# Optimization experiments

Hardware: AMD Instinct MI355X
Metric: run time of the kernel (lower is better)

Reference implementation:

```python
import jax, jax.numpy as jnp
import numpy as np

BATCH, SEQ, DMODEL, NSTATE = 4, 2048, 1024, 16


def setup_inputs() -> dict:
    key = jax.random.key(0)
    ks = jax.random.split(key, 6)
    def lin_w(k, out_d, in_d):
        # torch Linear default init scale ~ 1/sqrt(in_d)
        return jax.random.uniform(k, (out_d, in_d), jnp.float32, -1.0, 1.0) / np.sqrt(in_d).astype(np.float32)
    return {
        "x": jax.random.normal(ks[0], (BATCH, SEQ, DMODEL), jnp.float32),
        "W1": lin_w(ks[1], DMODEL, DMODEL), "b1": jnp.zeros((DMODEL,), jnp.float32),
        "W2": lin_w(ks[2], NSTATE, DMODEL), "b2": jnp.zeros((NSTATE,), jnp.float32),
        "W3": lin_w(ks[3], NSTATE, DMODEL), "b3": jnp.zeros((NSTATE,), jnp.float32),
        # A: xavier_uniform over (d_model, state_size)
        "A": jax.random.uniform(ks[4], (DMODEL, NSTATE), jnp.float32, -1.0, 1.0) * np.sqrt(6.0 / (DMODEL + NSTATE)).astype(np.float32),
    }


def reference(x, W1, b1, W2, b2, W3, b3, A):
    # Projections (bld -> bln / bld)
    Bmat = x @ W2.T + b2                      # (b, l, n)
    Cmat = x @ W3.T + b3                      # (b, l, n)
    delta = jax.nn.softplus(x @ W1.T + b1)    # (b, l, d)
    # Original math (flag=0 path):
    #   dB[b,l,d,n] = delta[b,l,d] * B[b,l,n]
    #   dA = exp(einsum('bld,dn->bldn', delta, A))  -- multiplied by a zeros h, so it
    #        contributes nothing to the output (dead math; A receives zero grad).
    #   h  = dA * 0 + x[...,None] * dB
    #   y  = einsum('bln,bldn->bld', C, h)
    # This reduces exactly to: y = x * delta * sum_n(B * C)
    bc = jnp.einsum('bln,bln->bl', Bmat, Cmat)  # (b, l)
    y = x * delta * bc[..., None]               # (b, l, d)
    return y
```

## Files before the change

kernel.cpp:

```cpp
#include <hip/hip_runtime.h>
#include <hip/hip_bf16.h>
#include <cmath>

#define BATCH 4
#define SEQ 2048
#define DM 1024
#define NS 16
#define M_ROWS (BATCH * SEQ)

typedef short bf16x8 __attribute__((ext_vector_type(8)));
typedef short bf16x4 __attribute__((ext_vector_type(4)));
typedef float f32x4 __attribute__((ext_vector_type(4)));

__device__ __forceinline__ short f2bf(float f) {
    union { float f; unsigned u; } a; a.f = f;
    unsigned u = a.u;
    return (short)((u + 0x7fffu + ((u >> 16) & 1u)) >> 16);
}
__device__ __forceinline__ float bf2f(unsigned short s) {
    union { unsigned u; float f; } a; a.u = ((unsigned)s) << 16;
    return a.f;
}

#define LDS_CAST(p) ((__attribute__((address_space(3))) unsigned*)(p))
#define GLB_CAST(p) ((const __attribute__((address_space(1))) unsigned*)(p))

__global__ void __launch_bounds__(256) convert_all(
    const float* __restrict__ x,  const float* __restrict__ W1,
    const float* __restrict__ W2, const float* __restrict__ W3,
    short* __restrict__ xb, short* __restrict__ W1b, short* __restrict__ Wcb)
{
    const int b = blockIdx.x;
    const int t = threadIdx.x;
    const float4* src; bf16x4* dst; int qbase;
    if (b < 2048)      { src = (const float4*)x;  dst = (bf16x4*)xb;  qbase = b * 1024; }
    else if (b < 2304) { src = (const float4*)W1; dst = (bf16x4*)W1b; qbase = (b - 2048) * 1024; }
    else if (b < 2308) { src = (const float4*)W2; dst = (bf16x4*)Wcb; qbase = (b - 2304) * 1024; }
    else               { src = (const float4*)W3; dst = (bf16x4*)(Wcb + NS * DM); qbase = (b - 2308) * 1024; }
    #pragma unroll
    for (int i = 0; i < 4; i++) {
        int q = qbase + i * 256 + t;
        float4 v = src[q];
        bf16x4 s;
        s.x = f2bf(v.x); s.y = f2bf(v.y); s.z = f2bf(v.z); s.w = f2bf(v.w);
        dst[q] = s;
    }
}

__global__ void __launch_bounds__(256, 4) gemm_fused(
    const short* __restrict__ xb, const short* __restrict__ W1b,
    const short* __restrict__ Wcb, const float* __restrict__ b1,
    const float* __restrict__ b2,  const float* __restrict__ b3,
    float* __restrict__ out)
{
    __shared__ short As[64][64];
    __shared__ short Bs[128][64];
    __shared__ short Wcs[32][64];
    __shared__ float bcs[64];

    const int n0 = blockIdx.x * 128;
    const int m0 = blockIdx.y * 64;
    const int t = threadIdx.x;
    const int lane = t & 63;
    const int w = t >> 6;
    const int wn = w * 32;
    const int lm = lane & 15;
    const int quad = lane >> 4;

    const int sr  = t >> 3;
    const int sc  = t & 7;
    const int gch = (sc ^ (sr & 7)) * 8;

    const short* pa = xb  + (size_t)(m0 + sr) * DM + gch;
    const short* pb = W1b + (size_t)(n0 + sr) * DM + gch;
    const short* pw = Wcb + (size_t)sr        * DM + gch;

    f32x4 acc[4][2] = {};
    f32x4 abc[2]    = {};

    #pragma unroll
    for (int kk = 0; kk < 16; kk++) {
        const int ke = kk * 64;
        #pragma unroll
        for (int u = 0; u < 2; u++)
            __builtin_amdgcn_global_load_lds(GLB_CAST(pa + (size_t)(u * 32) * DM + ke),
                LDS_CAST(&As[u * 32 + sr][sc * 8]), 16, 0, 0);
        #pragma unroll
        for (int u = 0; u < 4; u++)
            __builtin_amdgcn_global_load_lds(GLB_CAST(pb + (size_t)(u * 32) * DM + ke),
                LDS_CAST(&Bs[u * 32 + sr][sc * 8]), 16, 0, 0);
        __builtin_amdgcn_global_load_lds(GLB_CAST(pw + ke),
            LDS_CAST(&Wcs[sr][sc * 8]), 16, 0, 0);
        __syncthreads();

        #pragma unroll
        for (int ks = 0; ks < 2; ks++) {
            const int cs = ((ks * 4 + quad) ^ (lm & 7)) * 8;
            bf16x8 af[4], bfv[2], wcv[2];
            #pragma unroll
            for (int i = 0; i < 4; i++)
                af[i] = *(const bf16x8*)&As[i * 16 + lm][cs];
            #pragma unroll
            for (int j = 0; j < 2; j++)
                bfv[j] = *(const bf16x8*)&Bs[wn + j * 16 + lm][cs];
            #pragma unroll
            for (int h = 0; h < 2; h++)
                wcv[h] = *(const bf16x8*)&Wcs[h * 16 + lm][cs];

            #pragma unroll
            for (int i = 0; i < 4; i++)
                #pragma unroll
                for (int j = 0; j < 2; j++)
                    acc[i][j] = __builtin_amdgcn_mfma_f32_16x16x32_bf16(
                        af[i], bfv[j], acc[i][j], 0, 0, 0);

            if (w == 0) {
                abc[0] = __builtin_amdgcn_mfma_f32_16x16x32_bf16(af[0], wcv[0], abc[0], 0, 0, 0);
                abc[1] = __builtin_amdgcn_mfma_f32_16x16x32_bf16(af[0], wcv[1], abc[1], 0, 0, 0);
            } else if (w == 1) {
                abc[0] = __builtin_amdgcn_mfma_f32_16x16x32_bf16(af[1], wcv[0], abc[0], 0, 0, 0);
                abc[1] = __builtin_amdgcn_mfma_f32_16x16x32_bf16(af[1], wcv[1], abc[1], 0, 0, 0);
            } else if (w == 2) {
                abc[0] = __builtin_amdgcn_mfma_f32_16x16x32_bf16(af[2], wcv[0], abc[0], 0, 0, 0);
                abc[1] = __builtin_amdgcn_mfma_f32_16x16x32_bf16(af[2], wcv[1], abc[1], 0, 0, 0);
            } else {
                abc[0] = __builtin_amdgcn_mfma_f32_16x16x32_bf16(af[3], wcv[0], abc[0], 0, 0, 0);
                abc[1] = __builtin_amdgcn_mfma_f32_16x16x32_bf16(af[3], wcv[1], abc[1], 0, 0, 0);
            }
        }
        __syncthreads();
    }

    float bb2 = b2[lm], bb3 = b3[lm];
    #pragma unroll
    for (int r = 0; r < 4; r++) {
        float p = (abc[0][r] + bb2) * (abc[1][r] + bb3);
        p += __shfl_xor(p, 1);
        p += __shfl_xor(p, 2);
        p += __shfl_xor(p, 4);
        p += __shfl_xor(p, 8);
        if (lm == 0) bcs[w * 16 + quad * 4 + r] = p;
    }
    __syncthreads();

    const unsigned short* xbu = (const unsigned short*)xb;
    float b1v[2];
    #pragma unroll
    for (int j = 0; j < 2; j++) b1v[j] = b1[n0 + wn + j * 16 + lm];

    #pragma unroll
    for (int i = 0; i < 4; i++) {
        #pragma unroll
        for (int r = 0; r < 4; r++) {
            int lrow = i * 16 + quad * 4 + r;
            int gm = m0 + lrow;
            float bcv = bcs[lrow];
            const unsigned short* xrow = xbu + (size_t)gm * DM + n0 + wn + lm;
            float* orow = out + (size_t)gm * DM + n0 + wn + lm;
            #pragma unroll
            for (int j = 0; j < 2; j++) {
                float z = acc[i][j][r] + b1v[j];
                float az = __builtin_fabsf(z);
                float sp = fmaxf(z, 0.f) + __logf(1.f + __expf(-az));
                orow[j * 16] = bf2f(xrow[j * 16]) * sp * bcv;
            }
        }
    }
}

extern "C" void kernel_launch(void* const* d_in, const int* in_sizes, int n_in,
                              void* d_out, int out_size, void* d_ws, size_t ws_size,
                              hipStream_t stream) {
    const float* x  = (const float*)d_in[0];
    const float* W1 = (const float*)d_in[1];
    const float* b1 = (const float*)d_in[2];
    const float* W2 = (const float*)d_in[3];
    const float* b2 = (const float*)d_in[4];
    const float* W3 = (const float*)d_in[5];
    const float* b3 = (const float*)d_in[6];
    float* out = (float*)d_out;

    char* ws = (char*)d_ws;
    short* xb  = (short*)(ws);
    short* W1b = (short*)(ws + (size_t)16 * 1024 * 1024);
    short* Wcb = (short*)(ws + (size_t)18 * 1024 * 1024);

    convert_all<<<2312, 256, 0, stream>>>(x, W1, W2, W3, xb, W1b, Wcb);

    dim3 grid(DM / 128, M_ROWS / 64);
    gemm_fused<<<grid, 256, 0, stream>>>(xb, W1b, Wcb, b1, b2, b3, out);
}
```

Measured before the change: 128.1 us.

## Halve GEMM N-tile to 64 and load B/C projection weights directly from global

Shrinks the output tile per block from 64x128 to 64x64, doubling the grid and raising the occupancy hint to 6 blocks per CU, and drops the shared-memory staging of the W2/W3 weights in favour of direct per-lane global loads. The goal is more blocks in flight and less LDS traffic per block. The cost is that the x tile is reloaded twice as often and the small B/C projection is recomputed by twice as many blocks, adding redundant MFMA and global-load work.

Result: slower. 183.2 us (+43.0%).

```diff
diff --git a/kernel.cpp b/kernel.cpp
--- a/kernel.cpp
+++ b/kernel.cpp
@@ -47,23 +47,22 @@
     }
 }
 
-__global__ void __launch_bounds__(256, 4) gemm_fused(
+__global__ void __launch_bounds__(256, 6) gemm_fused(
     const short* __restrict__ xb, const short* __restrict__ W1b,
     const short* __restrict__ Wcb, const float* __restrict__ b1,
     const float* __restrict__ b2,  const float* __restrict__ b3,
     float* __restrict__ out)
 {
     __shared__ short As[64][64];
-    __shared__ short Bs[128][64];
-    __shared__ short Wcs[32][64];
+    __shared__ short Bs[64][64];
     __shared__ float bcs[64];
 
-    const int n0 = blockIdx.x * 128;
+    const int n0 = blockIdx.x * 64;
     const int m0 = blockIdx.y * 64;
     const int t = threadIdx.x;
     const int lane = t & 63;
     const int w = t >> 6;
-    const int wn = w * 32;
+    const int wn = w * 16;
     const int lm = lane & 15;
     const int quad = lane >> 4;
 
@@ -73,10 +72,11 @@
 
     const short* pa = xb  + (size_t)(m0 + sr) * DM + gch;
     const short* pb = W1b + (size_t)(n0 + sr) * DM + gch;
-    const short* pw = Wcb + (size_t)sr        * DM + gch;
+    const short* pW0 = Wcb + (size_t)(lm) * DM + quad * 8;
+    const short* pW1 = Wcb + (size_t)(16 + lm) * DM + quad * 8;
 
-    f32x4 acc[4][2] = {};
-    f32x4 abc[2]    = {};
+    f32x4 acc[4] = {};
+    f32x4 abc[2] = {};
 
     #pragma unroll
     for (int kk = 0; kk < 16; kk++) {
@@ -86,33 +86,27 @@
             __builtin_amdgcn_global_load_lds(GLB_CAST(pa + (size_t)(u * 32) * DM + ke),
                 LDS_CAST(&As[u * 32 + sr][sc * 8]), 16, 0, 0);
         #pragma unroll
-        for (int u = 0; u < 4; u++)
+        for (int u = 0; u < 2; u++)
             __builtin_amdgcn_global_load_lds(GLB_CAST(pb + (size_t)(u * 32) * DM + ke),
                 LDS_CAST(&Bs[u * 32 + sr][sc * 8]), 16, 0, 0);
-        __builtin_amdgcn_global_load_lds(GLB_CAST(pw + ke),
-            LDS_CAST(&Wcs[sr][sc * 8]), 16, 0, 0);
         __syncthreads();
 
         #pragma unroll
         for (int ks = 0; ks < 2; ks++) {
             const int cs = ((ks * 4 + quad) ^ (lm & 7)) * 8;
-            bf16x8 af[4], bfv[2], wcv[2];
+            const int eo = kk * 64 + ks * 32;
+            bf16x8 af[4], bfv, wcv[2];
             #pragma unroll
             for (int i = 0; i < 4; i++)
                 af[i] = *(const bf16x8*)&As[i * 16 + lm][cs];
-            #pragma unroll
-            for (int j = 0; j < 2; j++)
-                bfv[j] = *(const bf16x8*)&Bs[wn + j * 16 + lm][cs];
-            #pragma unroll
-            for (int h = 0; h < 2; h++)
-                wcv[h] = *(const bf16x8*)&Wcs[h * 16 + lm][cs];
+            bfv = *(const bf16x8*)&Bs[wn + lm][cs];
+            wcv[0] = *(const bf16x8*)(pW0 + eo);
+            wcv[1] = *(const bf16x8*)(pW1 + eo);
 
             #pragma unroll
             for (int i = 0; i < 4; i++)
-                #pragma unroll
-                for (int j = 0; j < 2; j++)
-                    acc[i][j] = __builtin_amdgcn_mfma_f32_16x16x32_bf16(
-                        af[i], bfv[j], acc[i][j], 0, 0, 0);
+                acc[i] = __builtin_amdgcn_mfma_f32_16x16x32_bf16(
+                    af[i], bfv, acc[i], 0, 0, 0);
 
             if (w == 0) {
                 abc[0] = __builtin_amdgcn_mfma_f32_16x16x32_bf16(af[0], wcv[0], abc[0], 0, 0, 0);
@@ -144,9 +138,7 @@
     __syncthreads();
 
     const unsigned short* xbu = (const unsigned short*)xb;
-    float b1v[2];
-    #pragma unroll
-    for (int j = 0; j < 2; j++) b1v[j] = b1[n0 + wn + j * 16 + lm];
+    const float b1v = b1[n0 + wn + lm];
 
     #pragma unroll
     for (int i = 0; i < 4; i++) {
@@ -155,15 +147,11 @@
             int lrow = i * 16 + quad * 4 + r;
             int gm = m0 + lrow;
             float bcv = bcs[lrow];
-            const unsigned short* xrow = xbu + (size_t)gm * DM + n0 + wn + lm;
-            float* orow = out + (size_t)gm * DM + n0 + wn + lm;
-            #pragma unroll
-            for (int j = 0; j < 2; j++) {
-                float z = acc[i][j][r] + b1v[j];
-                float az = __builtin_fabsf(z);
-                float sp = fmaxf(z, 0.f) + __logf(1.f + __expf(-az));
-                orow[j * 16] = bf2f(xrow[j * 16]) * sp * bcv;
-            }
+            float z = acc[i][r] + b1v;
+            float az = __builtin_fabsf(z);
+            float sp = fmaxf(z, 0.f) + __logf(1.f + __expf(-az));
+            size_t off = (size_t)gm * DM + n0 + wn + lm;
+            out[off] = bf2f(xbu[off]) * sp * bcv;
         }
     }
 }
@@ -187,6 +175,6 @@
 
     convert_all<<<2312, 256, 0, stream>>>(x, W1, W2, W3, xb, W1b, Wcb);
 
-    dim3 grid(DM / 128, M_ROWS / 64);
+    dim3 grid(DM / 64, M_ROWS / 64);
     gemm_fused<<<grid, 256, 0, stream>>>(xb, W1b, Wcb, b1, b2, b3, out);
 }
```
